# Optimization experiments

Measured on AMD Instinct MI355X. Metric: run time of the kernel, lower is better.

Reference implementation:

```python
import jax, jax.numpy as jnp
import numpy as np

DIM = 768
NUM_HEADS = 12
HEAD_DIM = DIM // NUM_HEADS
SCALE = HEAD_DIM ** -0.5


def setup_inputs() -> dict:
    key = jax.random.key(0)
    k1, k2, k3, k4, k5 = jax.random.split(key, 5)
    B, N, C = 4, 2048, DIM
    x = jax.random.normal(k1, (B, N, C), dtype=jnp.float32)
    xpos = jax.random.randint(k2, (B, N), 0, 2048, dtype=jnp.int32)
    # torch Linear weights: qkv (no bias), proj (with bias)
    lim_qkv = (1.0 / C) ** 0.5
    w_qkv = jax.random.uniform(k3, (3 * C, C), minval=-lim_qkv, maxval=lim_qkv, dtype=jnp.float32)
    w_proj = jax.random.uniform(k4, (C, C), minval=-lim_qkv, maxval=lim_qkv, dtype=jnp.float32)
    b_proj = jax.random.uniform(k5, (C,), minval=-lim_qkv, maxval=lim_qkv, dtype=jnp.float32)
    return {"x": x, "xpos": xpos, "w_qkv": w_qkv, "w_proj": w_proj, "b_proj": b_proj}


def reference(x, xpos, w_qkv, w_proj, b_proj):
    B, N, C = x.shape
    H, Dh = NUM_HEADS, HEAD_DIM
    # fused QKV projection: [B,N,3C] -> [B,N,3,H,Dh] -> [B,H,3,N,Dh]
    qkv = (x @ w_qkv.T).reshape(B, N, 3, H, Dh).transpose(0, 3, 2, 1, 4)
    q, k, v = qkv[:, :, 0], qkv[:, :, 1], qkv[:, :, 2]
    # rope is None -> xpos unused
    # naive attention: materialize full [B,H,N,N] scores (matches pytorch_naive)
    scores = jnp.einsum('bhqd,bhkd->bhqk', q, k) * SCALE
    attn = jax.nn.softmax(scores, axis=-1)
    out = jnp.einsum('bhqk,bhkd->bhqd', attn, v)  # [B,H,N,Dh]
    out = out.transpose(0, 2, 1, 3).reshape(B, N, C)
    return out @ w_proj.T + b_proj
```

## Files before the change

### kernel.cpp

```cpp
#include <hip/hip_runtime.h>
#include <math.h>

typedef __bf16 bf16;
typedef __attribute__((ext_vector_type(4))) __bf16 bf16x4;
typedef __attribute__((ext_vector_type(8))) __bf16 bf16x8;
typedef __attribute__((ext_vector_type(4))) float f32x4;

#define AS1 __attribute__((address_space(1)))
#define AS3 __attribute__((address_space(3)))

__device__ __forceinline__ void gload16(const void* g, void* l) {
  __builtin_amdgcn_global_load_lds((const AS1 void*)g, (AS3 void*)l, 16, 0, 0);
}

#define DIM 768
#define NH  12
#define HD  64
#define B_  4
#define N_  2048
#define M_  (B_*N_)
#define BH_ (B_*NH)

__global__ void convert_all(const float4* __restrict__ x,
                            const float4* __restrict__ wq,
                            const float4* __restrict__ wp,
                            bf16x4* __restrict__ xb,
                            bf16x4* __restrict__ wqb,
                            bf16x4* __restrict__ wpb) {
  const int nx = M_*DIM/4, nq = 3*DIM*DIM/4, np = DIM*DIM/4;
  const int total = nx + nq + np;
  for (int i = blockIdx.x*blockDim.x + threadIdx.x; i < total;
       i += gridDim.x*blockDim.x) {
    float4 v; bf16x4* dst;
    if (i < nx)           { v = x[i];         dst = xb  + i;         }
    else if (i < nx + nq) { v = wq[i-nx];     dst = wqb + (i-nx);    }
    else                  { v = wp[i-nx-nq];  dst = wpb + (i-nx-nq); }
    bf16x4 o = { (bf16)v.x, (bf16)v.y, (bf16)v.z, (bf16)v.w };
    *dst = o;
  }
}

template<int EPI>
__global__ __launch_bounds__(256)
void gemm_bt(const bf16* __restrict__ A, const bf16* __restrict__ B,
             bf16* __restrict__ qv, bf16* __restrict__ kv_, bf16* __restrict__ vt,
             const float* __restrict__ bprj, float* __restrict__ out) {
  constexpr int K = DIM;
  __shared__ __align__(16) bf16 As[128*32];
  __shared__ __align__(16) bf16 Bs[128*32];
  const int tid = threadIdx.x;
  const int wave = tid >> 6, lane = tid & 63;
  const int l15 = lane & 15, lg = lane >> 4;
  const int wr = wave >> 1, wc = wave & 1;
  const int m0 = blockIdx.y * 128, n0 = blockIdx.x * 128;

  f32x4 acc[4][4] = {};
  const int pbase = wave*2048 + lane*16;

  for (int kb = 0; kb < K; kb += 32) {
    __syncthreads();
#pragma unroll
    for (int i = 0; i < 2; i++) {
      int p = pbase + i*1024;
      int row = p >> 6, cb = p & 63;
      gload16((const char*)A + ((size_t)(m0+row)*K + kb)*2 + cb, (char*)As + p);
      gload16((const char*)B + ((size_t)(n0+row)*K + kb)*2 + cb, (char*)Bs + p);
    }
    __syncthreads();
    bf16x8 af[4], bfr[4];
#pragma unroll
    for (int f = 0; f < 4; f++) {
      af[f]  = *(const bf16x8*)(As + (wr*64 + f*16 + l15)*32 + lg*8);
      bfr[f] = *(const bf16x8*)(Bs + (wc*64 + f*16 + l15)*32 + lg*8);
    }
#pragma unroll
    for (int fm = 0; fm < 4; fm++)
#pragma unroll
      for (int fn = 0; fn < 4; fn++)
        acc[fm][fn] = __builtin_amdgcn_mfma_f32_16x16x32_bf16(af[fm], bfr[fn],
                                                              acc[fm][fn], 0, 0, 0);
  }

  if (EPI == 0) {
    const int c0 = n0 + wc*64;
    const int t = c0 / DIM;
    const int hcol = (c0 % DIM) >> 6;
#pragma unroll
    for (int fm = 0; fm < 4; fm++) {
      const int gm0 = m0 + wr*64 + fm*16 + (lg<<2);
      const int b = gm0 >> 11, nn0 = gm0 & 2047;
      const size_t bh = (size_t)b*NH + hcol;
#pragma unroll
      for (int fn = 0; fn < 4; fn++) {
        const int d = fn*16 + l15;
        if (t == 0) {
#pragma unroll
          for (int r = 0; r < 4; r++)
            qv[(bh*N_ + nn0 + r)*HD + d] = (bf16)(acc[fm][fn][r] * 0.125f);
        } else if (t == 1) {
#pragma unroll
          for (int r = 0; r < 4; r++)
            kv_[(bh*N_ + nn0 + r)*HD + d] = (bf16)acc[fm][fn][r];
        } else {
          bf16x4 pk = { (bf16)acc[fm][fn][0], (bf16)acc[fm][fn][1],
                        (bf16)acc[fm][fn][2], (bf16)acc[fm][fn][3] };
          *(bf16x4*)(vt + (bh*HD + d)*N_ + nn0) = pk;
        }
      }
    }
  } else {
#pragma unroll
    for (int fn = 0; fn < 4; fn++) {
      const int c = n0 + wc*64 + fn*16 + l15;
      const float bias = bprj[c];
#pragma unroll
      for (int fm = 0; fm < 4; fm++) {
        const int gm0 = m0 + wr*64 + fm*16 + (lg<<2);
#pragma unroll
        for (int r = 0; r < 4; r++)
          out[(size_t)(gm0 + r)*DIM + c] = acc[fm][fn][r] + bias;
      }
    }
  }
}

__global__ __launch_bounds__(256)
void attn_fwd(const bf16* __restrict__ Q, const bf16* __restrict__ Kb,
              const bf16* __restrict__ Vt, bf16* __restrict__ AO) {
  __shared__ __align__(16) bf16 Ks[64*64];
  __shared__ __align__(16) bf16 Vs[64*64];
  __shared__ __align__(16) bf16 Ps[4*32*64];
  const int tid = threadIdx.x;
  const int wave = tid >> 6, lane = tid & 63;
  const int l15 = lane & 15, lg = lane >> 4;
  const int bh = blockIdx.y;
  const int b = bh / NH, h = bh % NH;
  const int q0 = blockIdx.x*128 + wave*32;

  const bf16* Qbase = Q + (size_t)bh*N_*HD;
  bf16x8 qf[2][2];
#pragma unroll
  for (int fq = 0; fq < 2; fq++)
#pragma unroll
    for (int ks = 0; ks < 2; ks++)
      qf[fq][ks] = *(const bf16x8*)(Qbase + (size_t)(q0 + fq*16 + l15)*HD + ks*32 + lg*8);

  f32x4 O[2][4] = {};
  float mrow[2][4], lrow[2][4];
#pragma unroll
  for (int fq = 0; fq < 2; fq++)
#pragma unroll
    for (int r = 0; r < 4; r++) { mrow[fq][r] = -INFINITY; lrow[fq][r] = 0.f; }

  bf16* Pw = Ps + wave*32*64;
  const char* Kg = (const char*)(Kb + (size_t)bh*N_*HD);
  const char* Vg = (const char*)(Vt + (size_t)bh*HD*N_);
  const int pbase = wave*2048 + lane*16;

  for (int kv = 0; kv < N_; kv += 64) {
    __syncthreads();
#pragma unroll
    for (int i = 0; i < 2; i++) {
      int p = pbase + i*1024;
      int r = p >> 7, cbp = p & 127;
      int cb = cbp ^ ((r & 7) << 4);
      gload16(Kg + (size_t)(kv + r)*128 + cb, (char*)Ks + p);
      gload16(Vg + (size_t)r*(N_*2) + kv*2 + cb, (char*)Vs + p);
    }
    __syncthreads();

    f32x4 s[2][4] = {};
#pragma unroll
    for (int ks = 0; ks < 2; ks++) {
      bf16x8 kf[4];
#pragma unroll
      for (int fk = 0; fk < 4; fk++) {
        int r = fk*16 + l15;
        int cb = (ks*64 + lg*16) ^ ((r & 7) << 4);
        kf[fk] = *(const bf16x8*)((const char*)Ks + r*128 + cb);
      }
#pragma unroll
      for (int fq = 0; fq < 2; fq++)
#pragma unroll
        for (int fk = 0; fk < 4; fk++)
          s[fq][fk] = __builtin_amdgcn_mfma_f32_16x16x32_bf16(qf[fq][ks], kf[fk],
                                                              s[fq][fk], 0, 0, 0);
    }

#pragma unroll
    for (int fq = 0; fq < 2; fq++)
#pragma unroll
      for (int r = 0; r < 4; r++) {
        float mx = fmaxf(fmaxf(s[fq][0][r], s[fq][1][r]),
                         fmaxf(s[fq][2][r], s[fq][3][r]));
        mx = fmaxf(mx, __shfl_xor(mx, 1));
        mx = fmaxf(mx, __shfl_xor(mx, 2));
        mx = fmaxf(mx, __shfl_xor(mx, 4));
        mx = fmaxf(mx, __shfl_xor(mx, 8));
        const float mn = fmaxf(mrow[fq][r], mx);
        const float c = __expf(mrow[fq][r] - mn);
        mrow[fq][r] = mn;
        const int row = fq*16 + (lg<<2) + r;
        float rs = 0.f;
#pragma unroll
        for (int fk = 0; fk < 4; fk++) {
          float p = __expf(s[fq][fk][r] - mn);
          rs += p;
          int cb = ((fk*16 + l15) << 1) ^ ((row & 7) << 4);
          *(bf16*)((char*)Pw + row*128 + cb) = (bf16)p;
        }
        rs += __shfl_xor(rs, 1);
        rs += __shfl_xor(rs, 2);
        rs += __shfl_xor(rs, 4);
        rs += __shfl_xor(rs, 8);
        lrow[fq][r] = lrow[fq][r]*c + rs;
#pragma unroll
        for (int fd = 0; fd < 4; fd++) O[fq][fd][r] *= c;
      }

#pragma unroll
    for (int ks = 0; ks < 2; ks++) {
      bf16x8 pa[2];
#pragma unroll
      for (int fq = 0; fq < 2; fq++) {
        int row = fq*16 + l15;
        int cb = (ks*64 + lg*16) ^ ((row & 7) << 4);
        pa[fq] = *(const bf16x8*)((const char*)Pw + row*128 + cb);
      }
      bf16x8 vb[4];
#pragma unroll
      for (int fd = 0; fd < 4; fd++) {
        int r = fd*16 + l15;
        int cb = (ks*64 + lg*16) ^ ((r & 7) << 4);
        vb[fd] = *(const bf16x8*)((const char*)Vs + r*128 + cb);
      }
#pragma unroll
      for (int fq = 0; fq < 2; fq++)
#pragma unroll
        for (int fd = 0; fd < 4; fd++)
          O[fq][fd] = __builtin_amdgcn_mfma_f32_16x16x32_bf16(pa[fq], vb[fd],
                                                              O[fq][fd], 0, 0, 0);
    }
  }

#pragma unroll
  for (int fq = 0; fq < 2; fq++)
#pragma unroll
    for (int r = 0; r < 4; r++) {
      const float inv = 1.f / lrow[fq][r];
      const int nn = q0 + fq*16 + (lg<<2) + r;
#pragma unroll
      for (int fd = 0; fd < 4; fd++) {
        const int d = fd*16 + l15;
        AO[((size_t)b*N_ + nn)*DIM + h*HD + d] = (bf16)(O[fq][fd][r] * inv);
      }
    }
}

extern "C" void kernel_launch(void* const* d_in, const int* in_sizes, int n_in,
                              void* d_out, int out_size, void* d_ws, size_t ws_size,
                              hipStream_t stream) {
  const float* x     = (const float*)d_in[0];
  const float* wqkv  = (const float*)d_in[2];
  const float* wproj = (const float*)d_in[3];
  const float* bproj = (const float*)d_in[4];
  float* out = (float*)d_out;

  char* ws = (char*)d_ws;
  bf16* xb    = (bf16*)ws;  ws += (size_t)M_*DIM*2;
  bf16* wqkvb = (bf16*)ws;  ws += (size_t)3*DIM*DIM*2;
  bf16* wprojb= (bf16*)ws;  ws += (size_t)DIM*DIM*2;
  bf16* qb    = (bf16*)ws;  ws += (size_t)BH_*N_*HD*2;
  bf16* kb    = (bf16*)ws;  ws += (size_t)BH_*N_*HD*2;
  bf16* vtb   = (bf16*)ws;  ws += (size_t)BH_*HD*N_*2;
  bf16* aob   = (bf16*)ws;  ws += (size_t)M_*DIM*2;

  convert_all<<<dim3(2048), dim3(256), 0, stream>>>(
      (const float4*)x, (const float4*)wqkv, (const float4*)wproj,
      (bf16x4*)xb, (bf16x4*)wqkvb, (bf16x4*)wprojb);

  gemm_bt<0><<<dim3(3*DIM/128, M_/128), dim3(256), 0, stream>>>(
      xb, wqkvb, qb, kb, vtb, nullptr, nullptr);

  attn_fwd<<<dim3(N_/128, BH_), dim3(256), 0, stream>>>(qb, kb, vtb, aob);

  gemm_bt<1><<<dim3(DIM/128, M_/128), dim3(256), 0, stream>>>(
      aob, wprojb, nullptr, nullptr, nullptr, bproj, out);
}
```

Measured before the change: 324.4 us.

## Double-buffer K/V tiles, transpose S to keep P in registers, lazy rescale

```diff
diff --git a/kernel.cpp b/kernel.cpp
--- a/kernel.cpp
+++ b/kernel.cpp
@@ -5,12 +5,19 @@
 typedef __attribute__((ext_vector_type(4))) __bf16 bf16x4;
 typedef __attribute__((ext_vector_type(8))) __bf16 bf16x8;
 typedef __attribute__((ext_vector_type(4))) float f32x4;
+typedef __attribute__((ext_vector_type(4))) unsigned int u32x4;
 
 #define AS1 __attribute__((address_space(1)))
 #define AS3 __attribute__((address_space(3)))
 
 __device__ __forceinline__ void gload16(const void* g, void* l) {
   __builtin_amdgcn_global_load_lds((const AS1 void*)g, (AS3 void*)l, 16, 0, 0);
+}
+
+__device__ __forceinline__ unsigned int pack2bf(float lo, float hi) {
+  union { unsigned int u; __bf16 h[2]; } w;
+  w.h[0] = (bf16)lo; w.h[1] = (bf16)hi;
+  return w.u;
 }
 
 #define DIM 768
@@ -127,9 +134,8 @@
 __global__ __launch_bounds__(256)
 void attn_fwd(const bf16* __restrict__ Q, const bf16* __restrict__ Kb,
               const bf16* __restrict__ Vt, bf16* __restrict__ AO) {
-  __shared__ __align__(16) bf16 Ks[64*64];
-  __shared__ __align__(16) bf16 Vs[64*64];
-  __shared__ __align__(16) bf16 Ps[4*32*64];
+  __shared__ __align__(16) bf16 Ks[2][64*64];
+  __shared__ __align__(16) bf16 Vs[2][64*64];
   const int tid = threadIdx.x;
   const int wave = tid >> 6, lane = tid & 63;
   const int l15 = lane & 15, lg = lane >> 4;
@@ -145,29 +151,35 @@
     for (int ks = 0; ks < 2; ks++)
       qf[fq][ks] = *(const bf16x8*)(Qbase + (size_t)(q0 + fq*16 + l15)*HD + ks*32 + lg*8);
 
-  f32x4 O[2][4] = {};
-  float mrow[2][4], lrow[2][4];
-#pragma unroll
-  for (int fq = 0; fq < 2; fq++)
-#pragma unroll
-    for (int r = 0; r < 4; r++) { mrow[fq][r] = -INFINITY; lrow[fq][r] = 0.f; }
-
-  bf16* Pw = Ps + wave*32*64;
+  f32x4 Ot[2][4] = {};
+  float m_[2] = { -INFINITY, -INFINITY };
+  float l_[2] = { 0.f, 0.f };
+
   const char* Kg = (const char*)(Kb + (size_t)bh*N_*HD);
   const char* Vg = (const char*)(Vt + (size_t)bh*HD*N_);
   const int pbase = wave*2048 + lane*16;
-
-  for (int kv = 0; kv < N_; kv += 64) {
+  const bool lower = (lane < 32);
+  const bool q03 = (lg == 0) || (lg == 3);
+
+#define STAGE(buf, kv)                                                      \
+  {                                                                         \
+    _Pragma("unroll")                                                       \
+    for (int i = 0; i < 2; i++) {                                           \
+      int p = pbase + i*1024;                                               \
+      int r = p >> 7, cbp = p & 127;                                        \
+      int cb = cbp ^ ((r & 7) << 4);                                        \
+      gload16(Kg + (size_t)((kv) + r)*128 + cb, (char*)Ks[buf] + p);        \
+      gload16(Vg + (size_t)r*(N_*2) + (kv)*2 + cb, (char*)Vs[buf] + p);     \
+    }                                                                       \
+  }
+
+  STAGE(0, 0);
+
+  for (int t = 0; t < N_/64; ++t) {
     __syncthreads();
-#pragma unroll
-    for (int i = 0; i < 2; i++) {
-      int p = pbase + i*1024;
-      int r = p >> 7, cbp = p & 127;
-      int cb = cbp ^ ((r & 7) << 4);
-      gload16(Kg + (size_t)(kv + r)*128 + cb, (char*)Ks + p);
-      gload16(Vg + (size_t)r*(N_*2) + kv*2 + cb, (char*)Vs + p);
-    }
-    __syncthreads();
+    if (t + 1 < N_/64) STAGE((t+1)&1, (t+1)*64);
+    const char* Kc = (const char*)Ks[t&1];
+    const char* Vc = (const char*)Vs[t&1];
 
     f32x4 s[2][4] = {};
 #pragma unroll
@@ -177,84 +189,115 @@
       for (int fk = 0; fk < 4; fk++) {
         int r = fk*16 + l15;
         int cb = (ks*64 + lg*16) ^ ((r & 7) << 4);
-        kf[fk] = *(const bf16x8*)((const char*)Ks + r*128 + cb);
+        kf[fk] = *(const bf16x8*)(Kc + r*128 + cb);
       }
 #pragma unroll
       for (int fq = 0; fq < 2; fq++)
 #pragma unroll
         for (int fk = 0; fk < 4; fk++)
-          s[fq][fk] = __builtin_amdgcn_mfma_f32_16x16x32_bf16(qf[fq][ks], kf[fk],
+          s[fq][fk] = __builtin_amdgcn_mfma_f32_16x16x32_bf16(kf[fk], qf[fq][ks],
                                                               s[fq][fk], 0, 0, 0);
     }
 
-#pragma unroll
-    for (int fq = 0; fq < 2; fq++)
-#pragma unroll
-      for (int r = 0; r < 4; r++) {
-        float mx = fmaxf(fmaxf(s[fq][0][r], s[fq][1][r]),
-                         fmaxf(s[fq][2][r], s[fq][3][r]));
-        mx = fmaxf(mx, __shfl_xor(mx, 1));
-        mx = fmaxf(mx, __shfl_xor(mx, 2));
-        mx = fmaxf(mx, __shfl_xor(mx, 4));
-        mx = fmaxf(mx, __shfl_xor(mx, 8));
-        const float mn = fmaxf(mrow[fq][r], mx);
-        const float c = __expf(mrow[fq][r] - mn);
-        mrow[fq][r] = mn;
-        const int row = fq*16 + (lg<<2) + r;
-        float rs = 0.f;
-#pragma unroll
-        for (int fk = 0; fk < 4; fk++) {
-          float p = __expf(s[fq][fk][r] - mn);
-          rs += p;
-          int cb = ((fk*16 + l15) << 1) ^ ((row & 7) << 4);
-          *(bf16*)((char*)Pw + row*128 + cb) = (bf16)p;
-        }
-        rs += __shfl_xor(rs, 1);
-        rs += __shfl_xor(rs, 2);
-        rs += __shfl_xor(rs, 4);
-        rs += __shfl_xor(rs, 8);
-        lrow[fq][r] = lrow[fq][r]*c + rs;
-#pragma unroll
-        for (int fd = 0; fd < 4; fd++) O[fq][fd][r] *= c;
-      }
+    unsigned int paw[2][2][4];
+#pragma unroll
+    for (int fq = 0; fq < 2; fq++) {
+      float mx = s[fq][0][0];
+#pragma unroll
+      for (int fk = 0; fk < 4; fk++)
+#pragma unroll
+        for (int r = 0; r < 4; r++) mx = fmaxf(mx, s[fq][fk][r]);
+      mx = fmaxf(mx, __shfl_xor(mx, 16));
+      mx = fmaxf(mx, __shfl_xor(mx, 32));
+      if (!__all(mx - m_[fq] <= 6.0f)) {
+        float mn = fmaxf(m_[fq], mx);
+        float c = __expf(m_[fq] - mn);
+        m_[fq] = mn; l_[fq] *= c;
+#pragma unroll
+        for (int fd = 0; fd < 4; fd++) Ot[fq][fd] *= c;
+      }
+      float pe[4][4]; float rs = 0.f;
+#pragma unroll
+      for (int fk = 0; fk < 4; fk++)
+#pragma unroll
+        for (int r = 0; r < 4; r++) {
+          pe[fk][r] = __expf(s[fq][fk][r] - m_[fq]);
+          rs += pe[fk][r];
+        }
+      rs += __shfl_xor(rs, 16);
+      rs += __shfl_xor(rs, 32);
+      l_[fq] += rs;
+
+      unsigned int pk[4][2];
+#pragma unroll
+      for (int fk = 0; fk < 4; fk++)
+#pragma unroll
+        for (int rp = 0; rp < 2; rp++)
+          pk[fk][rp] = pack2bf(pe[fk][2*rp], pe[fk][2*rp+1]);
+
+      unsigned int Eo[2][2], Er[2][2], rB[2][2];
+#pragma unroll
+      for (int fh = 0; fh < 2; fh++)
+#pragma unroll
+        for (int rp = 0; rp < 2; rp++) {
+          unsigned int vA = lower ? pk[2*fh+1][rp] : pk[2*fh][rp];
+          Er[fh][rp] = __shfl_xor((int)vA, 32);
+          Eo[fh][rp] = lower ? pk[2*fh][rp] : pk[2*fh+1][rp];
+        }
+#pragma unroll
+      for (int fh = 0; fh < 2; fh++)
+#pragma unroll
+        for (int rp = 0; rp < 2; rp++) {
+          unsigned int vB = q03 ? Er[fh][rp] : Eo[fh][rp];
+          rB[fh][rp] = __shfl_xor((int)vB, 16);
+        }
+#pragma unroll
+      for (int ks = 0; ks < 2; ks++) {
+#pragma unroll
+        for (int rp = 0; rp < 2; rp++) {
+          paw[fq][ks][rp] = (lg == 0) ? Eo[ks][rp] :
+                            (lg == 1) ? rB[ks][rp] :
+                            (lg == 2) ? Er[ks][rp] : rB[ks][rp];
+          paw[fq][ks][2+rp] = (lg == 0) ? rB[ks][rp] :
+                              (lg == 1) ? Er[ks][rp] :
+                              (lg == 2) ? rB[ks][rp] : Eo[ks][rp];
+        }
+      }
+    }
 
 #pragma unroll
     for (int ks = 0; ks < 2; ks++) {
-      bf16x8 pa[2];
-#pragma unroll
-      for (int fq = 0; fq < 2; fq++) {
-        int row = fq*16 + l15;
-        int cb = (ks*64 + lg*16) ^ ((row & 7) << 4);
-        pa[fq] = *(const bf16x8*)((const char*)Pw + row*128 + cb);
-      }
       bf16x8 vb[4];
 #pragma unroll
       for (int fd = 0; fd < 4; fd++) {
         int r = fd*16 + l15;
         int cb = (ks*64 + lg*16) ^ ((r & 7) << 4);
-        vb[fd] = *(const bf16x8*)((const char*)Vs + r*128 + cb);
-      }
-#pragma unroll
-      for (int fq = 0; fq < 2; fq++)
+        vb[fd] = *(const bf16x8*)(Vc + r*128 + cb);
+      }
+#pragma unroll
+      for (int fq = 0; fq < 2; fq++) {
+        u32x4 tw = { paw[fq][ks][0], paw[fq][ks][1], paw[fq][ks][2], paw[fq][ks][3] };
+        bf16x8 pa = __builtin_bit_cast(bf16x8, tw);
 #pragma unroll
         for (int fd = 0; fd < 4; fd++)
-          O[fq][fd] = __builtin_amdgcn_mfma_f32_16x16x32_bf16(pa[fq], vb[fd],
-                                                              O[fq][fd], 0, 0, 0);
-    }
-  }
-
-#pragma unroll
-  for (int fq = 0; fq < 2; fq++)
-#pragma unroll
-    for (int r = 0; r < 4; r++) {
-      const float inv = 1.f / lrow[fq][r];
-      const int nn = q0 + fq*16 + (lg<<2) + r;
-#pragma unroll
-      for (int fd = 0; fd < 4; fd++) {
-        const int d = fd*16 + l15;
-        AO[((size_t)b*N_ + nn)*DIM + h*HD + d] = (bf16)(O[fq][fd][r] * inv);
-      }
-    }
+          Ot[fq][fd] = __builtin_amdgcn_mfma_f32_16x16x32_bf16(vb[fd], pa,
+                                                               Ot[fq][fd], 0, 0, 0);
+      }
+    }
+  }
+
+#pragma unroll
+  for (int fq = 0; fq < 2; fq++) {
+    const float inv = 1.f / l_[fq];
+    const int qrow = q0 + fq*16 + l15;
+#pragma unroll
+    for (int fd = 0; fd < 4; fd++) {
+      bf16x4 pk4 = { (bf16)(Ot[fq][fd][0]*inv), (bf16)(Ot[fq][fd][1]*inv),
+                     (bf16)(Ot[fq][fd][2]*inv), (bf16)(Ot[fq][fd][3]*inv) };
+      *(bf16x4*)(AO + ((size_t)b*N_ + qrow)*DIM + h*HD + fd*16 + lg*4) = pk4;
+    }
+  }
+#undef STAGE
 }
 
 extern "C" void kernel_launch(void* const* d_in, const int* in_sizes, int n_in,
```

New measurement: 267.2 us. 1.21x faster.
